# Kernel tuning notes

Measured on AMD Instinct MI355X. Metric: run time of the kernel, lower is better.

## Reference

```python
import math
import jax, jax.numpy as jnp
import numpy as np

N_EMBD = 1024
N_HEAD = 16
NUM_BUCKETS = 32
MAX_DISTANCE = 128


def _relative_position_bucket(relative_position, num_buckets=NUM_BUCKETS, max_distance=MAX_DISTANCE):
    # unidirectional (bidirectional=False): rp = -min(rp, 0)
    rp = -jnp.minimum(relative_position, 0)
    max_exact = num_buckets // 2
    is_small = rp < max_exact
    rp_large = max_exact + (
        jnp.log(rp.astype(jnp.float32) / max_exact + 1e-10)
        / math.log(max_distance / max_exact)
        * (num_buckets - max_exact)
    ).astype(jnp.int32)
    rp_large = jnp.minimum(rp_large, num_buckets - 1)
    return jnp.where(is_small, rp, rp_large)


def setup_inputs() -> dict:
    key = jax.random.key(0)
    ks = jax.random.split(key, 6)
    B, T, C = 4, 2048, N_EMBD
    s_in = 1.0 / math.sqrt(C)
    x = jax.random.normal(ks[0], (B, T, C), dtype=jnp.float32)
    W_attn = jax.random.normal(ks[1], (3 * C, C), dtype=jnp.float32) * s_in
    b_attn = jnp.zeros((3 * C,), dtype=jnp.float32)
    W_proj = jax.random.normal(ks[2], (C, C), dtype=jnp.float32) * s_in
    b_proj = jnp.zeros((C,), dtype=jnp.float32)
    rel_emb = jax.random.normal(ks[3], (NUM_BUCKETS, N_HEAD), dtype=jnp.float32) * 0.02
    return {"x": x, "W_attn": W_attn, "b_attn": b_attn,
            "W_proj": W_proj, "b_proj": b_proj, "rel_emb": rel_emb}


def reference(x, W_attn, b_attn, W_proj, b_proj, rel_emb):
    B, T, C = x.shape
    H = N_HEAD
    D = C // H
    qkv = x @ W_attn.T + b_attn              # [B,T,3C]
    q, k, v = jnp.split(qkv, 3, axis=-1)
    q = q.reshape(B, T, H, D).transpose(0, 2, 1, 3)  # [B,H,T,D]
    k = k.reshape(B, T, H, D).transpose(0, 2, 1, 3)
    v = v.reshape(B, T, H, D).transpose(0, 2, 1, 3)

    # T5 relative position bias (unidirectional)
    pos = jnp.arange(T)
    rel_pos = pos[None, :] - pos[:, None]            # [T,T] key - query
    buckets = _relative_position_bucket(rel_pos)     # [T,T]
    rel_bias = rel_emb[buckets]                      # [T,T,H]
    rel_bias = rel_bias.transpose(2, 0, 1)[None]     # [1,H,T,T]

    att = jnp.einsum('bhqd,bhkd->bhqk', q, k) * (1.0 / math.sqrt(D))
    att = att + rel_bias
    causal = jnp.tril(jnp.ones((T, T), dtype=bool))
    att = jnp.where(causal[None, None], att, -jnp.inf)
    att = jax.nn.softmax(att, axis=-1)
    y = jnp.einsum('bhqk,bhkd->bhqd', att, v)        # [B,H,T,D]
    y = y.transpose(0, 2, 1, 3).reshape(B, T, C)
    y = y @ W_proj.T + b_proj
    return y
```

## Files before the change

kernel.cpp:

```cpp
#include <hip/hip_runtime.h>
#include <hip/hip_bf16.h>

typedef __attribute__((ext_vector_type(8))) short short8;
typedef __attribute__((ext_vector_type(4))) short short4v;
typedef __attribute__((ext_vector_type(4))) float f32x4;

#define DEVI static __device__ __forceinline__

#define MTOK 8192
#define CDIM 1024
#define HN 16
#define HD 64
#define TSEQ 2048

#if defined(__has_builtin)
#if __has_builtin(__builtin_amdgcn_exp2f)
#define EXP2(x) __builtin_amdgcn_exp2f(x)
#else
#define EXP2(x) exp2f(x)
#endif
#else
#define EXP2(x) exp2f(x)
#endif

DEVI short bf16_rne(float f) {
  union { float f; unsigned u; } v; v.f = f;
  unsigned r = v.u + 0x7FFFu + ((v.u >> 16) & 1u);
  return (short)(r >> 16);
}

DEVI void gload16(const void* g, void* l) {
  __builtin_amdgcn_global_load_lds(
      (const __attribute__((address_space(1))) void*)(unsigned long long)g,
      (__attribute__((address_space(3))) void*)(unsigned long long)l, 16, 0, 0);
}

#define MFMA_B16(A,B,C) __builtin_amdgcn_mfma_f32_16x16x32_bf16(A,B,C,0,0,0)

__global__ void pack_kernel(const float* __restrict__ x, const float* __restrict__ Wa,
                            const float* __restrict__ Wp,
                            short* __restrict__ xb, short* __restrict__ wab,
                            short* __restrict__ wpb) {
  const int NX4 = MTOK*CDIM/4, NA4 = 3*CDIM*CDIM/4, NP4 = CDIM*CDIM/4;
  const int total = NX4 + NA4 + NP4;
  for (int i = blockIdx.x*blockDim.x + threadIdx.x; i < total; i += gridDim.x*blockDim.x) {
    const float* src; short* dst; int off;
    if (i < NX4)          { src = x;  dst = xb;  off = i*4; }
    else if (i < NX4+NA4) { src = Wa; dst = wab; off = (i-NX4)*4; }
    else                  { src = Wp; dst = wpb; off = (i-NX4-NA4)*4; }
    float4 v = *(const float4*)(src + off);
    short4v r;
    r.x = bf16_rne(v.x); r.y = bf16_rne(v.y); r.z = bf16_rne(v.z); r.w = bf16_rne(v.w);
    *(short4v*)(dst + off) = r;
  }
}

__global__ void bias_table_kernel(const float* __restrict__ rel_emb, float* __restrict__ tab) {
  int d = blockIdx.x*blockDim.x + threadIdx.x;
  if (d >= TSEQ) return;
  int bucket;
  if (d < 16) bucket = d;
  else {
    int bl = 16 + (int)(logf((float)d / 16.0f + 1e-10f) / 2.0794415416798357f * 16.0f);
    bucket = bl < 31 ? bl : 31;
  }
  for (int h = 0; h < HN; h++) tab[h*TSEQ + d] = rel_emb[bucket*HN + h];
}

template<int EPI>
__global__ __launch_bounds__(256)
void gemm_bt(const short* __restrict__ A, const short* __restrict__ B,
             const float* __restrict__ bias,
             short* __restrict__ oq, short* __restrict__ ok, short* __restrict__ ov,
             float* __restrict__ of) {
  const int K = CDIM;
  int nbx = gridDim.x;
  int idx = blockIdx.y * nbx + blockIdx.x;
  int cpx = (nbx * gridDim.y) >> 3;
  int sw = (idx & 7) * cpx + (idx >> 3);
  int n0 = (sw % nbx) * 128, m0 = (sw / nbx) * 128;

  int tid = threadIdx.x;
  int lane = tid & 63, w = tid >> 6;
  int wr = w >> 1, wc = w & 1;
  int r16 = lane & 15, g = lane >> 4;

  __shared__ __align__(16) short As[128*32];
  __shared__ __align__(16) short Bs[128*32];

  f32x4 zf = {0.f, 0.f, 0.f, 0.f};
  f32x4 acc[4][4];
  #pragma unroll
  for (int m = 0; m < 4; m++)
    #pragma unroll
    for (int n = 0; n < 4; n++) acc[m][n] = zf;

  int sr = tid >> 2;
  int sc = (tid & 3) * 8;
  const short* ga = A + (long long)(m0 + sr) * K + sc;
  const short* gb = B + (long long)(n0 + sr) * K + sc;
  short* la = As + sr*32 + sc;
  short* lb = Bs + sr*32 + sc;

  for (int k0 = 0; k0 < K; k0 += 32) {
    gload16(ga + k0,           la);
    gload16(ga + k0 + 64*K,    la + 64*32);
    gload16(gb + k0,           lb);
    gload16(gb + k0 + 64*K,    lb + 64*32);
    __syncthreads();
    short8 af[4], bfv[4];
    #pragma unroll
    for (int m = 0; m < 4; m++)
      af[m] = *(const short8*)&As[(wr*64 + m*16 + r16)*32 + g*8];
    #pragma unroll
    for (int n = 0; n < 4; n++)
      bfv[n] = *(const short8*)&Bs[(wc*64 + n*16 + r16)*32 + g*8];
    #pragma unroll
    for (int m = 0; m < 4; m++)
      #pragma unroll
      for (int n = 0; n < 4; n++)
        acc[m][n] = MFMA_B16(af[m], bfv[n], acc[m][n]);
    __syncthreads();
  }

  #pragma unroll
  for (int mi = 0; mi < 4; mi++) {
    #pragma unroll
    for (int n = 0; n < 4; n++) {
      int col = n0 + wc*64 + n*16 + r16;
      float bv = bias[col];
      if constexpr (EPI == 0) {
        int which = col >> 10;
        int c = col & (CDIM-1);
        int hh = c >> 6, dd = c & 63;
        short* outp = (which == 0) ? oq : (which == 1) ? ok : ov;
        #pragma unroll
        for (int j = 0; j < 4; j++) {
          int row = m0 + wr*64 + mi*16 + g*4 + j;
          int b = row >> 11, t = row & (TSEQ-1);
          outp[(((long long)(b*HN + hh))*TSEQ + t)*HD + dd] = bf16_rne(acc[mi][n][j] + bv);
        }
      } else {
        #pragma unroll
        for (int j = 0; j < 4; j++) {
          int row = m0 + wr*64 + mi*16 + g*4 + j;
          of[(long long)row*CDIM + col] = acc[mi][n][j] + bv;
        }
      }
    }
  }
}

__global__ __launch_bounds__(256)
void vtrans_kernel(const short* __restrict__ vin, short* __restrict__ vout) {
  int bh = blockIdx.x >> 5;
  int t0 = (blockIdx.x & 31) * 64;
  __shared__ short tile[64][72];
  int tid = threadIdx.x;
  const short* src = vin + ((long long)bh*TSEQ + t0)*HD;
  #pragma unroll
  for (int i = 0; i < 2; i++) {
    int idx = tid + i*256;
    int r = idx >> 3, c = (idx & 7)*8;
    short8 v = *(const short8*)(src + r*HD + c);
    #pragma unroll
    for (int j = 0; j < 8; j++) tile[r][c+j] = v[j];
  }
  __syncthreads();
  short* dst = vout + (long long)bh*HD*TSEQ + t0;
  #pragma unroll
  for (int i = 0; i < 2; i++) {
    int idx = tid + i*256;
    int d = idx >> 3, c = (idx & 7)*8;
    short8 v;
    #pragma unroll
    for (int j = 0; j < 8; j++) v[j] = tile[c+j][d];
    *(short8*)(dst + (long long)d*TSEQ + c) = v;
  }
}

__global__ __launch_bounds__(256)
void attn_kernel(const short* __restrict__ Qg, const short* __restrict__ Kg,
                 const short* __restrict__ Vtg, const float* __restrict__ btab,
                 short* __restrict__ outp) {
  int bh = blockIdx.x;
  int qb = 15 - (int)blockIdx.y;
  int h = bh & (HN-1), b = bh >> 4;
  int q0 = qb * 128;
  int tid = threadIdx.x, lane = tid & 63, w = tid >> 6;
  int r16 = lane & 15, g = lane >> 4;

  __shared__ __align__(16) short Ks[64*64];
  __shared__ __align__(16) short Vs[64*64];
  __shared__ __align__(16) short Ps[8][1024];
  __shared__ float bias_s[TSEQ];

  for (int i = tid; i < TSEQ; i += 256) bias_s[i] = btab[h*TSEQ + i] * 1.44269504f;

  short8 qa[2][2];
  #pragma unroll
  for (int mi = 0; mi < 2; mi++)
    #pragma unroll
    for (int ks = 0; ks < 2; ks++)
      qa[mi][ks] = *(const short8*)(Qg + ((long long)bh*TSEQ + q0 + w*32 + mi*16 + r16)*HD + ks*32 + g*8);

  f32x4 zf = {0.f,0.f,0.f,0.f};
  f32x4 o[2][4];
  #pragma unroll
  for (int mi = 0; mi < 2; mi++)
    #pragma unroll
    for (int c = 0; c < 4; c++) o[mi][c] = zf;
  float m_[2] = {-1e30f, -1e30f}, l_[2] = {0.f, 0.f};

  int qmax_wave = q0 + w*32 + 31;
  int swz = r16 & 7;
  int qrel = q0 + w*32 + r16;
  const float SC = 0.18033688f;

  for (int kb = 0; kb < q0 + 128; kb += 64) {
    #pragma unroll
    for (int i = 0; i < 2; i++) {
      int idx = tid + i*256;
      int r = idx >> 3;
      int cq = ((idx & 7) ^ (r & 7)) * 8;
      gload16(Kg  + ((long long)bh*TSEQ + kb + r)*HD + cq, (short*)Ks + idx*8);
      gload16(Vtg + ((long long)bh*HD  + r)*TSEQ + kb + cq, (short*)Vs + idx*8);
    }
    __syncthreads();
    if (kb <= qmax_wave) {
      f32x4 s[2][4];
      #pragma unroll
      for (int mi = 0; mi < 2; mi++)
        #pragma unroll
        for (int n = 0; n < 4; n++) s[mi][n] = zf;
      #pragma unroll
      for (int n = 0; n < 4; n++) {
        #pragma unroll
        for (int ks = 0; ks < 2; ks++) {
          short8 kf = *(const short8*)&Ks[(n*16 + r16)*64 + ((ks*4 + g) ^ swz)*8];
          s[0][n] = MFMA_B16(kf, qa[0][ks], s[0][n]);
          s[1][n] = MFMA_B16(kf, qa[1][ks], s[1][n]);
        }
      }
      #pragma unroll
      for (int mi = 0; mi < 2; mi++) {
        int dbase = qrel + mi*16 - kb - g*4;
        float rowv[4][4];
        #pragma unroll
        for (int n = 0; n < 4; n++)
          #pragma unroll
          for (int j = 0; j < 4; j++) {
            int d = dbase - n*16 - j;
            rowv[n][j] = (d >= 0) ? s[mi][n][j]*SC + bias_s[d] : -1e30f;
          }
        float mx = rowv[0][0];
        #pragma unroll
        for (int n = 0; n < 4; n++)
          #pragma unroll
          for (int j = 0; j < 4; j++) mx = fmaxf(mx, rowv[n][j]);
        mx = fmaxf(mx, __shfl_xor(mx, 16));
        mx = fmaxf(mx, __shfl_xor(mx, 32));
        float mnew = fmaxf(m_[mi], mx);
        float corr = EXP2(m_[mi] - mnew);
        m_[mi] = mnew;
        float ps_ = 0.f;
        unsigned pk[4][2];
        #pragma unroll
        for (int n = 0; n < 4; n++) {
          #pragma unroll
          for (int jj = 0; jj < 2; jj++) {
            float p0 = EXP2(rowv[n][jj*2]   - mnew);
            float p1 = EXP2(rowv[n][jj*2+1] - mnew);
            ps_ += p0 + p1;
            pk[n][jj] = ((unsigned)(unsigned short)bf16_rne(p1) << 16) |
                        (unsigned)(unsigned short)bf16_rne(p0);
          }
        }
        ps_ += __shfl_xor(ps_, 16);
        ps_ += __shfl_xor(ps_, 32);
        l_[mi] = l_[mi]*corr + ps_;
        #pragma unroll
        for (int c = 0; c < 4; c++) o[mi][c] *= corr;
        char* prow = (char*)Ps[w*2 + mi] + r16*128 + ((g & 1) << 3);
        #pragma unroll
        for (int n = 0; n < 4; n++)
          *(uint2*)(prow + ((((n*2 + (g >> 1)) ^ swz)) << 4)) = make_uint2(pk[n][0], pk[n][1]);
      }
      #pragma unroll
      for (int ks = 0; ks < 2; ks++) {
        short8 pf0 = *(const short8*)((char*)Ps[w*2+0] + r16*128 + (((ks*4 + g) ^ swz) << 4));
        short8 pf1 = *(const short8*)((char*)Ps[w*2+1] + r16*128 + (((ks*4 + g) ^ swz) << 4));
        #pragma unroll
        for (int c = 0; c < 4; c++) {
          short8 vf = *(const short8*)&Vs[(c*16 + r16)*64 + ((ks*4 + g) ^ swz)*8];
          o[0][c] = MFMA_B16(vf, pf0, o[0][c]);
          o[1][c] = MFMA_B16(vf, pf1, o[1][c]);
        }
      }
    }
    __syncthreads();
  }

  #pragma unroll
  for (int mi = 0; mi < 2; mi++) {
    float inv = 1.0f / l_[mi];
    long long base = ((long long)(b*TSEQ + qrel + mi*16))*CDIM + h*HD;
    #pragma unroll
    for (int c = 0; c < 4; c++) {
      #pragma unroll
      for (int jj = 0; jj < 2; jj++) {
        unsigned pv = ((unsigned)(unsigned short)bf16_rne(o[mi][c][jj*2+1]*inv) << 16) |
                      (unsigned)(unsigned short)bf16_rne(o[mi][c][jj*2]*inv);
        *(unsigned*)(outp + base + c*16 + g*4 + jj*2) = pv;
      }
    }
  }
}

extern "C" void kernel_launch(void* const* d_in, const int* in_sizes, int n_in,
                              void* d_out, int out_size, void* d_ws, size_t ws_size,
                              hipStream_t stream) {
  (void)in_sizes; (void)n_in; (void)out_size; (void)ws_size;
  const float* x      = (const float*)d_in[0];
  const float* W_attn = (const float*)d_in[1];
  const float* b_attn = (const float*)d_in[2];
  const float* W_proj = (const float*)d_in[3];
  const float* b_proj = (const float*)d_in[4];
  const float* rel    = (const float*)d_in[5];
  float* out = (float*)d_out;
  char* ws = (char*)d_ws;

  short* xb   = (short*)(ws);
  short* wab  = (short*)(ws + 16777216LL);
  short* wpb  = (short*)(ws + 23068672LL);
  short* qbuf = (short*)(ws + 25165824LL);
  short* kbuf = (short*)(ws + 41943040LL);
  short* vbuf = (short*)(ws + 58720256LL);
  short* att  = (short*)(ws + 75497472LL);
  float* tab  = (float*)(ws + 92274688LL);
  short* vt   = xb;

  pack_kernel<<<2048, 256, 0, stream>>>(x, W_attn, W_proj, xb, wab, wpb);
  bias_table_kernel<<<8, 256, 0, stream>>>(rel, tab);
  gemm_bt<0><<<dim3(24, 64), 256, 0, stream>>>(xb, wab, b_attn, qbuf, kbuf, vbuf, nullptr);
  vtrans_kernel<<<2048, 256, 0, stream>>>(vbuf, vt);
  attn_kernel<<<dim3(64, 16), 256, 0, stream>>>(qbuf, kbuf, vt, tab, att);
  gemm_bt<1><<<dim3(8, 64), 256, 0, stream>>>(att, wpb, b_proj, nullptr, nullptr, nullptr, out);
}
```

Before: 311.4 us.

## Streamline attention softmax: far-tile constant bias, lazy rescale, MFMA row sums

For key tiles far enough from the diagonal, the relative-position bias is constant (the last bucket), so the softmax skips the masking and bias lookup and uses a single fused multiply-add per score. The running-max rescale is skipped when the new max exceeds the old by at most 8 (in log2 units), row sums are computed with an MFMA against a ones vector rather than shuffles, and bf16 packing uses the hardware v_cvt_pk_bf16_f32 instruction. The bias table in shared memory shrinks to 256 entries and the V-transpose tile padding changes. This adds more code paths and relies on the threshold-based lazy max staying numerically safe.

```diff
diff --git a/kernel.cpp b/kernel.cpp
--- a/kernel.cpp
+++ b/kernel.cpp
@@ -27,6 +27,12 @@
   union { float f; unsigned u; } v; v.f = f;
   unsigned r = v.u + 0x7FFFu + ((v.u >> 16) & 1u);
   return (short)(r >> 16);
+}
+
+DEVI unsigned cvt_pk_bf16(float lo, float hi) {
+  unsigned r;
+  asm("v_cvt_pk_bf16_f32 %0, %1, %2" : "=v"(r) : "v"(lo), "v"(hi));
+  return r;
 }
 
 DEVI void gload16(const void* g, void* l) {
@@ -155,7 +161,7 @@
 void vtrans_kernel(const short* __restrict__ vin, short* __restrict__ vout) {
   int bh = blockIdx.x >> 5;
   int t0 = (blockIdx.x & 31) * 64;
-  __shared__ short tile[64][72];
+  __shared__ short tile[64][66];
   int tid = threadIdx.x;
   const short* src = vin + ((long long)bh*TSEQ + t0)*HD;
   #pragma unroll
@@ -193,9 +199,10 @@
   __shared__ __align__(16) short Ks[64*64];
   __shared__ __align__(16) short Vs[64*64];
   __shared__ __align__(16) short Ps[8][1024];
-  __shared__ float bias_s[TSEQ];
-
-  for (int i = tid; i < TSEQ; i += 256) bias_s[i] = btab[h*TSEQ + i] * 1.44269504f;
+  __shared__ float bias_s[256];
+
+  bias_s[tid & 255] = btab[h*TSEQ + (tid & 255)] * 1.44269504f;
+  float cb = btab[h*TSEQ + 255] * 1.44269504f;
 
   short8 qa[2][2];
   #pragma unroll
@@ -212,6 +219,7 @@
     for (int c = 0; c < 4; c++) o[mi][c] = zf;
   float m_[2] = {-1e30f, -1e30f}, l_[2] = {0.f, 0.f};
 
+  const short8 ones = {0x3f80,0x3f80,0x3f80,0x3f80,0x3f80,0x3f80,0x3f80,0x3f80};
   int qmax_wave = q0 + w*32 + 31;
   int swz = r16 & 7;
   int qrel = q0 + w*32 + r16;
@@ -242,54 +250,82 @@
           s[1][n] = MFMA_B16(kf, qa[1][ks], s[1][n]);
         }
       }
+      bool far = (kb + 176 <= q0 + w*32);
       #pragma unroll
       for (int mi = 0; mi < 2; mi++) {
-        int dbase = qrel + mi*16 - kb - g*4;
-        float rowv[4][4];
-        #pragma unroll
-        for (int n = 0; n < 4; n++)
-          #pragma unroll
-          for (int j = 0; j < 4; j++) {
-            int d = dbase - n*16 - j;
-            rowv[n][j] = (d >= 0) ? s[mi][n][j]*SC + bias_s[d] : -1e30f;
+        char* prow = (char*)Ps[w*2 + mi] + r16*128 + ((g & 1) << 3);
+        if (far) {
+          float smax = s[mi][0][0];
+          #pragma unroll
+          for (int n = 0; n < 4; n++)
+            #pragma unroll
+            for (int j = 0; j < 4; j++) smax = fmaxf(smax, s[mi][n][j]);
+          float mx = smax*SC + cb;
+          mx = fmaxf(mx, __shfl_xor(mx, 16));
+          mx = fmaxf(mx, __shfl_xor(mx, 32));
+          float mnew;
+          if (__all(mx <= m_[mi] + 8.0f)) {
+            mnew = m_[mi];
+          } else {
+            mnew = fmaxf(m_[mi], mx);
+            float corr = EXP2(m_[mi] - mnew);
+            l_[mi] *= corr;
+            #pragma unroll
+            for (int c = 0; c < 4; c++) o[mi][c] *= corr;
+            m_[mi] = mnew;
           }
-        float mx = rowv[0][0];
-        #pragma unroll
-        for (int n = 0; n < 4; n++)
-          #pragma unroll
-          for (int j = 0; j < 4; j++) mx = fmaxf(mx, rowv[n][j]);
-        mx = fmaxf(mx, __shfl_xor(mx, 16));
-        mx = fmaxf(mx, __shfl_xor(mx, 32));
-        float mnew = fmaxf(m_[mi], mx);
-        float corr = EXP2(m_[mi] - mnew);
-        m_[mi] = mnew;
-        float ps_ = 0.f;
-        unsigned pk[4][2];
-        #pragma unroll
-        for (int n = 0; n < 4; n++) {
-          #pragma unroll
-          for (int jj = 0; jj < 2; jj++) {
-            float p0 = EXP2(rowv[n][jj*2]   - mnew);
-            float p1 = EXP2(rowv[n][jj*2+1] - mnew);
-            ps_ += p0 + p1;
-            pk[n][jj] = ((unsigned)(unsigned short)bf16_rne(p1) << 16) |
-                        (unsigned)(unsigned short)bf16_rne(p0);
+          float cc = cb - mnew;
+          #pragma unroll
+          for (int n = 0; n < 4; n++) {
+            unsigned u0 = cvt_pk_bf16(EXP2(__builtin_fmaf(s[mi][n][0], SC, cc)),
+                                      EXP2(__builtin_fmaf(s[mi][n][1], SC, cc)));
+            unsigned u1 = cvt_pk_bf16(EXP2(__builtin_fmaf(s[mi][n][2], SC, cc)),
+                                      EXP2(__builtin_fmaf(s[mi][n][3], SC, cc)));
+            *(uint2*)(prow + ((((n*2 + (g >> 1)) ^ swz)) << 4)) = make_uint2(u0, u1);
           }
-        }
-        ps_ += __shfl_xor(ps_, 16);
-        ps_ += __shfl_xor(ps_, 32);
-        l_[mi] = l_[mi]*corr + ps_;
-        #pragma unroll
-        for (int c = 0; c < 4; c++) o[mi][c] *= corr;
-        char* prow = (char*)Ps[w*2 + mi] + r16*128 + ((g & 1) << 3);
-        #pragma unroll
-        for (int n = 0; n < 4; n++)
-          *(uint2*)(prow + ((((n*2 + (g >> 1)) ^ swz)) << 4)) = make_uint2(pk[n][0], pk[n][1]);
-      }
+        } else {
+          int dbase = qrel + mi*16 - kb - g*4;
+          float rowv[4][4];
+          #pragma unroll
+          for (int n = 0; n < 4; n++)
+            #pragma unroll
+            for (int j = 0; j < 4; j++) {
+              int d = dbase - n*16 - j;
+              rowv[n][j] = (d >= 0) ? s[mi][n][j]*SC + bias_s[d] : -1e30f;
+            }
+          float mx = rowv[0][0];
+          #pragma unroll
+          for (int n = 0; n < 4; n++)
+            #pragma unroll
+            for (int j = 0; j < 4; j++) mx = fmaxf(mx, rowv[n][j]);
+          mx = fmaxf(mx, __shfl_xor(mx, 16));
+          mx = fmaxf(mx, __shfl_xor(mx, 32));
+          float mnew;
+          if (__all(mx <= m_[mi] + 8.0f)) {
+            mnew = m_[mi];
+          } else {
+            mnew = fmaxf(m_[mi], mx);
+            float corr = EXP2(m_[mi] - mnew);
+            l_[mi] *= corr;
+            #pragma unroll
+            for (int c = 0; c < 4; c++) o[mi][c] *= corr;
+            m_[mi] = mnew;
+          }
+          #pragma unroll
+          for (int n = 0; n < 4; n++) {
+            unsigned u0 = cvt_pk_bf16(EXP2(rowv[n][0] - mnew), EXP2(rowv[n][1] - mnew));
+            unsigned u1 = cvt_pk_bf16(EXP2(rowv[n][2] - mnew), EXP2(rowv[n][3] - mnew));
+            *(uint2*)(prow + ((((n*2 + (g >> 1)) ^ swz)) << 4)) = make_uint2(u0, u1);
+          }
+        }
+      }
+      f32x4 lacc[2] = {zf, zf};
       #pragma unroll
       for (int ks = 0; ks < 2; ks++) {
         short8 pf0 = *(const short8*)((char*)Ps[w*2+0] + r16*128 + (((ks*4 + g) ^ swz) << 4));
         short8 pf1 = *(const short8*)((char*)Ps[w*2+1] + r16*128 + (((ks*4 + g) ^ swz) << 4));
+        lacc[0] = MFMA_B16(ones, pf0, lacc[0]);
+        lacc[1] = MFMA_B16(ones, pf1, lacc[1]);
         #pragma unroll
         for (int c = 0; c < 4; c++) {
           short8 vf = *(const short8*)&Vs[(c*16 + r16)*64 + ((ks*4 + g) ^ swz)*8];
@@ -297,6 +333,8 @@
           o[1][c] = MFMA_B16(vf, pf1, o[1][c]);
         }
       }
+      l_[0] += lacc[0][0];
+      l_[1] += lacc[1][0];
     }
     __syncthreads();
   }
@@ -309,8 +347,7 @@
     for (int c = 0; c < 4; c++) {
       #pragma unroll
       for (int jj = 0; jj < 2; jj++) {
-        unsigned pv = ((unsigned)(unsigned short)bf16_rne(o[mi][c][jj*2+1]*inv) << 16) |
-                      (unsigned)(unsigned short)bf16_rne(o[mi][c][jj*2]*inv);
+        unsigned pv = cvt_pk_bf16(o[mi][c][jj*2]*inv, o[mi][c][jj*2+1]*inv);
         *(unsigned*)(outp + base + c*16 + g*4 + jj*2) = pv;
       }
     }
```

Result: faster. 273.8 us (-12.1%).
